# Optimization experiments

Measured on AMD Instinct MI355X. Metric: run time of the kernel, lower is better.

The kernel has to match this reference:

```python
import jax, jax.numpy as jnp
import numpy as np

N, E, R = 50000, 400000, 500
X_SIZE = 100
G_SIZE = 100
HID = 64
OUT = 64
HEADS = 2
ALPHA = 0.5
NEG_SLOPE = 0.01  # nn.LeakyReLU default and attention slope
EPS = 1e-12       # F.normalize eps


def _l2norm(x, axis):
    return x / jnp.maximum(jnp.linalg.norm(x, axis=axis, keepdims=True), EPS)


def _xavier(key, shape, gain=1.414):
    fan_in, fan_out = shape[-1], int(np.prod(shape[:-1]))
    std = gain * np.sqrt(2.0 / (fan_in + fan_out))
    return jax.random.normal(key, shape, dtype=jnp.float32) * std


def _att_layer(h, g, row, col, etype, W, b, att, out_size):
    # h: [N, D_h], g: [R, D_g], W: [heads*out, 2*D_h+D_g], att: [1, heads, out]
    n = h.shape[0]
    h_ijk = jnp.concatenate([h[row], h[col], g[etype]], axis=1)      # [E, 2D_h+D_g]
    c_ijk = (h_ijk @ W.T + b).reshape(-1, HEADS, out_size)           # [E, H, O]
    a = jnp.sum(att * c_ijk, axis=2, keepdims=True)                  # [E, H, 1]
    e = jnp.exp(jax.nn.leaky_relu(a, NEG_SLOPE))                     # unnormalized (matches torch exp w/o max-sub)
    denom = jax.ops.segment_sum(e, row, num_segments=n)              # [N, H, 1]
    alpha = e / denom[row]
    # self-edge zeros contribute nothing; segment_sum over num_segments=n is equivalent
    return jax.ops.segment_sum(alpha * c_ijk, col, num_segments=n)   # [N, H, O]


def setup_inputs() -> dict:
    key = jax.random.key(0)
    ks = jax.random.split(key, 20)
    x = jax.random.normal(ks[0], (N, X_SIZE), dtype=jnp.float32)
    g = jax.random.normal(ks[1], (R, G_SIZE), dtype=jnp.float32)
    edge_idx = jax.random.randint(ks[2], (2, E), 0, N)
    edge_type = jax.random.randint(ks[3], (E,), 0, R)
    d1 = 2 * X_SIZE + G_SIZE
    d2 = 2 * HID * HEADS + G_SIZE
    inp = {
        "x": x, "g": g, "edge_idx": edge_idx, "edge_type": edge_type,
        "W1i": _xavier(ks[4], (HEADS * HID, d1)), "b1i": jnp.zeros((HEADS * HID,), jnp.float32),
        "a1i": _xavier(ks[5], (1, HEADS, HID)),
        "W1o": _xavier(ks[6], (HEADS * HID, d1)), "b1o": jnp.zeros((HEADS * HID,), jnp.float32),
        "a1o": _xavier(ks[7], (1, HEADS, HID)),
        "W2i": _xavier(ks[8], (HEADS * OUT, d2)), "b2i": jnp.zeros((HEADS * OUT,), jnp.float32),
        "a2i": _xavier(ks[9], (1, HEADS, OUT)),
        "W2o": _xavier(ks[10], (HEADS * OUT, d2)), "b2o": jnp.zeros((HEADS * OUT,), jnp.float32),
        "a2o": _xavier(ks[11], (1, HEADS, OUT)),
        "We": _xavier(ks[12], (HID, X_SIZE)), "be": jnp.zeros((HID,), jnp.float32),
        "Wr": _xavier(ks[13], (HEADS * HID, G_SIZE)), "br": jnp.zeros((HEADS * HID,), jnp.float32),
    }
    return inp


def reference(x, g, edge_idx, edge_type, W1i, b1i, a1i, W1o, b1o, a1o,
              W2i, b2i, a2i, W2o, b2o, a2o, We, be, Wr, br):
    # x = F.normalize(x, dim=1).detach()
    xn = jax.lax.stop_gradient(_l2norm(x, axis=1))
    row, col = edge_idx[0], edge_idx[1]

    h_in = _att_layer(xn, g, row, col, edge_type, W1i, b1i, a1i, HID)
    h_out = _att_layer(xn, g, col, row, edge_type, W1o, b1o, a1o, HID)
    h = jax.nn.leaky_relu(ALPHA * h_in + (1.0 - ALPHA) * h_out, NEG_SLOPE)
    h = _l2norm(h, axis=2)                                # [N, H, HID]
    h = h.transpose(0, 1, 2).reshape(N, HEADS * HID)      # concat heads

    h_in = _att_layer(h, g, row, col, edge_type, W2i, b2i, a2i, OUT)
    h_out = _att_layer(h, g, col, row, edge_type, W2o, b2o, a2o, OUT)
    h = jax.nn.leaky_relu(ALPHA * h_in + (1.0 - ALPHA) * h_out, NEG_SLOPE)
    h = _l2norm(h, axis=2)                                # [N, H, OUT]

    # EntityLayer: Linear(x)[:, None, :] + h  (requires HID == OUT)
    h_prime = (xn @ We.T + be)[:, None, :] + h            # [N, H, OUT]
    h_prime = h_prime.reshape(N, HEADS * OUT)
    h_prime = _l2norm(h_prime, axis=1)                    # (torch dim=2 bug -> last dim)
    # _merge_heads stores mean but returns input unchanged

    g_prime = g @ Wr.T + br                               # [R, HEADS*HID]
    return h_prime, g_prime
```

## Files before the change

### kernel.cpp

```cpp
#include <hip/hip_runtime.h>

typedef unsigned short u16;
typedef unsigned int u32;
typedef short short8v __attribute__((ext_vector_type(8)));
typedef float float4v __attribute__((ext_vector_type(4)));

#define N_NODES 50000
#define E_EDGES 400000
#define R_REL   500
#define NKEYS   100000
#define SCAN_B  98
#define SEG     ((size_t)N_NODES * 128)

__device__ __forceinline__ float bl(u32 u){ return __uint_as_float(u << 16); }
__device__ __forceinline__ float bh(u32 u){ return __uint_as_float(u & 0xffff0000u); }
__device__ __forceinline__ u16 f2b(float f){
    u32 u = __float_as_uint(f);
    return (u16)((u + 0x7fffu + ((u >> 16) & 1u)) >> 16);
}
__device__ __forceinline__ u32 pk2(float a, float b){ return (u32)f2b(a) | ((u32)f2b(b) << 16); }
__device__ __forceinline__ float lrelu(float x){ return x > 0.f ? x : 0.01f * x; }

__global__ void k_norm_x(const float* __restrict__ x, u16* __restrict__ xnb){
    int wid = threadIdx.x >> 6, l = threadIdx.x & 63;
    int n = blockIdx.x * 4 + wid;
    if (n >= N_NODES) return;
    float v0 = x[(size_t)n * 100 + l];
    float v1 = (l + 64 < 100) ? x[(size_t)n * 100 + 64 + l] : 0.f;
    float ss = v0 * v0 + v1 * v1;
    #pragma unroll
    for (int m = 32; m; m >>= 1) ss += __shfl_xor(ss, m);
    float s = 1.f / fmaxf(sqrtf(ss), 1e-12f);
    xnb[(size_t)n * 128 + l] = f2b(v0 * s);
    xnb[(size_t)n * 128 + 64 + l] = (l + 64 < 100) ? f2b(v1 * s) : (u16)0;
}

__global__ void k_build_wcat(const float* __restrict__ W1i, const float* __restrict__ W1o,
                             const float* __restrict__ W2i, const float* __restrict__ W2o,
                             const float* __restrict__ We,
                             const float* __restrict__ a1i, const float* __restrict__ a1o,
                             const float* __restrict__ a2i, const float* __restrict__ a2o,
                             u16* __restrict__ wc1, u16* __restrict__ wc2,
                             float* __restrict__ attcat){
    int idx = blockIdx.x * blockDim.x + threadIdx.x;
    if (idx < 576 * 128){
        int r = idx >> 7, k = idx & 127;
        float v = 0.f;
        if (r < 512){
            int seg = r >> 7, rr = r & 127;
            const float* W = (seg < 2) ? W1i : W1o;
            int off = (seg & 1) ? 100 : 0;
            if (k < 100) v = W[(size_t)rr * 300 + off + k];
        } else {
            int rr = r - 512;
            if (k < 100) v = We[(size_t)rr * 100 + k];
        }
        wc1[idx] = f2b(v);
    } else if (idx < 576 * 128 + 512 * 128){
        int j = idx - 576 * 128;
        int r = j >> 7, k = j & 127;
        int seg = r >> 7, rr = r & 127;
        const float* W = (seg < 2) ? W2i : W2o;
        int off = (seg & 1) ? 128 : 0;
        wc2[j] = f2b(W[(size_t)rr * 356 + off + k]);
    } else if (idx < 576 * 128 + 512 * 128 + 1024){
        int j = idx - (576 * 128 + 512 * 128);
        int s = j >> 9, cc = j & 511;
        const float* a = s ? ((cc < 256) ? a2i : a2o) : ((cc < 256) ? a1i : a1o);
        attcat[j] = a[cc & 127];
    }
}

__global__ void k_pg(const float* __restrict__ g,
                     const float* __restrict__ W1i, const float* __restrict__ W1o,
                     const float* __restrict__ W2i, const float* __restrict__ W2o,
                     const float* __restrict__ b1i, const float* __restrict__ b1o,
                     const float* __restrict__ b2i, const float* __restrict__ b2o,
                     const float* __restrict__ a1i, const float* __restrict__ a1o,
                     const float* __restrict__ a2i, const float* __restrict__ a2o,
                     float* __restrict__ Pg, float* __restrict__ qg){
    int bid = blockIdx.x;
    int r = bid >> 2, t = bid & 3;
    const float *W, *b, *att; int ld, off;
    if (t == 0){ W = W1i; ld = 300; off = 200; b = b1i; att = a1i; }
    else if (t == 1){ W = W1o; ld = 300; off = 200; b = b1o; att = a1o; }
    else if (t == 2){ W = W2i; ld = 356; off = 256; b = b2i; att = a2i; }
    else { W = W2o; ld = 356; off = 256; b = b2o; att = a2o; }
    __shared__ float gs[100];
    __shared__ float red[128];
    int j = threadIdx.x;
    if (j < 100) gs[j] = g[(size_t)r * 100 + j];
    __syncthreads();
    float acc = b[j];
    #pragma unroll 4
    for (int k = 0; k < 100; ++k) acc += gs[k] * W[(size_t)j * ld + off + k];
    Pg[((size_t)t * R_REL + r) * 128 + j] = acc;
    red[j] = att[j] * acc;
    __syncthreads();
    if (j < 2){
        float s = 0.f;
        for (int k = 0; k < 64; ++k) s += red[j * 64 + k];
        qg[((size_t)t * R_REL + r) * 2 + j] = s;
    }
}

__global__ void k_gprime(const float* __restrict__ g, const float* __restrict__ Wr,
                         const float* __restrict__ br, float* __restrict__ out){
    int r = blockIdx.x, j = threadIdx.x;
    __shared__ float gs[100];
    if (j < 100) gs[j] = g[(size_t)r * 100 + j];
    __syncthreads();
    float acc = br[j];
    #pragma unroll 4
    for (int k = 0; k < 100; ++k) acc += gs[k] * Wr[(size_t)j * 100 + k];
    out[(size_t)N_NODES * 128 + (size_t)r * 128 + j] = acc;
}

__launch_bounds__(256)
__global__ void k_gemm(const u16* __restrict__ A, const u16* __restrict__ W,
                       const float* __restrict__ attcat,
                       u16* __restrict__ NPt, float* __restrict__ q, int M, int NN){
    int l = threadIdx.x & 63, w = threadIdx.x >> 6;
    int rb = blockIdx.x * 64 + w * 16;
    int ar = rb + (l & 15); if (ar >= M) ar = M - 1;
    const u16* Ap = A + (size_t)ar * 128 + (l >> 4) * 8;
    short8v a0 = *(const short8v*)(Ap);
    short8v a1 = *(const short8v*)(Ap + 32);
    short8v a2 = *(const short8v*)(Ap + 64);
    short8v a3 = *(const short8v*)(Ap + 96);
    float qa[4] = {0.f, 0.f, 0.f, 0.f};
    int ntc = NN >> 4;
    for (int nt = 0; nt < ntc; ++nt){
        const u16* Wp = W + (size_t)(nt * 16 + (l & 15)) * 128 + (l >> 4) * 8;
        short8v b0 = *(const short8v*)(Wp);
        short8v b1 = *(const short8v*)(Wp + 32);
        short8v b2 = *(const short8v*)(Wp + 64);
        short8v b3 = *(const short8v*)(Wp + 96);
        float4v acc = {0.f, 0.f, 0.f, 0.f};
        acc = __builtin_amdgcn_mfma_f32_16x16x32_bf16(a0, b0, acc, 0, 0, 0);
        acc = __builtin_amdgcn_mfma_f32_16x16x32_bf16(a1, b1, acc, 0, 0, 0);
        acc = __builtin_amdgcn_mfma_f32_16x16x32_bf16(a2, b2, acc, 0, 0, 0);
        acc = __builtin_amdgcn_mfma_f32_16x16x32_bf16(a3, b3, acc, 0, 0, 0);
        int cc = nt * 16 + (l & 15);
        int seg = cc >> 7;
        int rr0 = rb + (l >> 4) * 4;
        #pragma unroll
        for (int r = 0; r < 4; ++r){
            int rr = rr0 + r;
            if (rr < M){
                if (seg < 4) NPt[(size_t)seg * SEG + (size_t)rr * 128 + (cc & 127)] = f2b(acc[r]);
                else         NPt[4 * SEG + (size_t)rr * 64 + (cc & 63)] = f2b(acc[r]);
            }
        }
        int g = nt >> 2;
        if (g < 8){
            float av = attcat[cc];
            #pragma unroll
            for (int r = 0; r < 4; ++r) qa[r] += av * acc[r];
            if ((nt & 3) == 3){
                #pragma unroll
                for (int r = 0; r < 4; ++r){
                    float s = qa[r];
                    s += __shfl_xor(s, 1); s += __shfl_xor(s, 2);
                    s += __shfl_xor(s, 4); s += __shfl_xor(s, 8);
                    if ((l & 15) == 0){
                        int rr = rr0 + r;
                        if (rr < M) q[(size_t)rr * 8 + g] = s;
                    }
                    qa[r] = 0.f;
                }
            }
        }
    }
}

__global__ void k_hist(const int* __restrict__ ei, u32* __restrict__ cnt){
    int e = blockIdx.x * blockDim.x + threadIdx.x;
    if (e >= E_EDGES) return;
    atomicAdd(&cnt[ei[E_EDGES + e]], 1u);
    atomicAdd(&cnt[N_NODES + ei[e]], 1u);
}

__launch_bounds__(1024)
__global__ void k_scan1(const u32* __restrict__ cnt, u32* __restrict__ off, u32* __restrict__ bsum){
    __shared__ u32 sh[1024];
    int t = threadIdx.x, b = blockIdx.x, idx = b * 1024 + t;
    u32 v = cnt[idx];
    sh[t] = v; __syncthreads();
    #pragma unroll
    for (int d = 1; d < 1024; d <<= 1){
        u32 add = (t >= d) ? sh[t - d] : 0;
        __syncthreads();
        sh[t] += add;
        __syncthreads();
    }
    off[idx] = sh[t] - v;
    if (t == 1023) bsum[b] = sh[1023];
}

__global__ void k_scan2(u32* __restrict__ bsum){
    if (threadIdx.x == 0){
        u32 run = 0;
        for (int i = 0; i < SCAN_B; ++i){ u32 t = bsum[i]; bsum[i] = run; run += t; }
    }
}

__launch_bounds__(1024)
__global__ void k_scan3(u32* __restrict__ off, const u32* __restrict__ bsum){
    int idx = blockIdx.x * 1024 + threadIdx.x;
    off[idx] += bsum[blockIdx.x];
}

__global__ void k_pos(const int* __restrict__ ei, const int* __restrict__ ety,
                      u32* __restrict__ cur,
                      u32* __restrict__ Pso, u32* __restrict__ Pss){
    int e = blockIdx.x * blockDim.x + threadIdx.x;
    if (e >= E_EDGES) return;
    u32 row = (u32)ei[e], col = (u32)ei[E_EDGES + e];
    u32 etb = (u32)ety[e] << 20;
    u32 pI = atomicAdd(&cur[col], 1u);
    Pso[pI] = row | etb;  Pss[pI] = col;
    u32 pO = atomicAdd(&cur[N_NODES + row], 1u);
    Pso[pO] = col | etb;  Pss[pO] = row;
}

__global__ void k_edgeA(const u32* __restrict__ Pso, const u32* __restrict__ Pss,
                        const float* __restrict__ q,
                        const float* __restrict__ qgI, const float* __restrict__ qgO,
                        float2* __restrict__ exI, float2* __restrict__ exO){
    int p = blockIdx.x * blockDim.x + threadIdx.x;
    if (p >= 2 * E_EDGES) return;
    u32 so = Pso[p], self = Pss[p];
    u32 oth = so & 0xFFFFF, et = so >> 20;
    u32 row, col;
    if (p < E_EDGES){ row = oth; col = self; } else { row = self; col = oth; }
    const float* qr = q + (size_t)row * 8;
    const float* qc = q + (size_t)col * 8;
    float2 ri, ro;
    ri.x = expf(lrelu(qr[0] + qc[2] + qgI[(size_t)et * 2 + 0]));
    ri.y = expf(lrelu(qr[1] + qc[3] + qgI[(size_t)et * 2 + 1]));
    ro.x = expf(lrelu(qc[4] + qr[6] + qgO[(size_t)et * 2 + 0]));
    ro.y = expf(lrelu(qc[5] + qr[7] + qgO[(size_t)et * 2 + 1]));
    exI[p] = ri;
    exO[p] = ro;
}

__global__ void k_denom(const u32* __restrict__ off,
                        const float2* __restrict__ exI, const float2* __restrict__ exO,
                        float* __restrict__ rdI, float* __restrict__ rdO){
    int n = blockIdx.x * blockDim.x + threadIdx.x;
    if (n >= N_NODES) return;
    float s0 = 0.f, s1 = 0.f;
    for (u32 p = off[N_NODES + n]; p < off[N_NODES + n + 1]; ++p){
        float2 v = exI[p]; s0 += v.x; s1 += v.y;
    }
    rdI[(size_t)n * 2 + 0] = (s0 > 0.f) ? 1.f / s0 : 0.f;
    rdI[(size_t)n * 2 + 1] = (s1 > 0.f) ? 1.f / s1 : 0.f;
    float t0 = 0.f, t1 = 0.f;
    for (u32 p = off[n]; p < off[n + 1]; ++p){
        float2 v = exO[p]; t0 += v.x; t1 += v.y;
    }
    rdO[(size_t)n * 2 + 0] = (t0 > 0.f) ? 1.f / t0 : 0.f;
    rdO[(size_t)n * 2 + 1] = (t1 > 0.f) ? 1.f / t1 : 0.f;
}

__launch_bounds__(256)
__global__ void k_agg(const u32* __restrict__ off,
                      const u32* __restrict__ Pso,
                      const float2* __restrict__ exI, const float2* __restrict__ exO,
                      const u16* __restrict__ NPt,
                      const float* __restrict__ PgI, const float* __restrict__ PgO,
                      const float* __restrict__ rdI, const float* __restrict__ rdO,
                      int final_stage,
                      const u16* __restrict__ NPt1, const float* __restrict__ be,
                      u16* __restrict__ h1b, float* __restrict__ out){
    int wid = threadIdx.x >> 6, l = threadIdx.x & 63;
    int n = blockIdx.x * 4 + wid;
    if (n >= N_NODES) return;
    int h = l >> 5, d0 = l * 2;
    const u16* PaI = NPt;
    const u16* PbI = NPt + SEG;
    const u16* PaO = NPt + 2 * SEG;
    const u16* PbO = NPt + 3 * SEG;
    u32 pbi = *(const u32*)(PbI + (size_t)n * 128 + d0);
    u32 pbo = *(const u32*)(PbO + (size_t)n * 128 + d0);

    float a0 = 0.f, a1 = 0.f, sai = 0.f;
    {
        u32 s0 = off[n], deg = off[n + 1] - s0;
        for (u32 base = 0; base < deg; base += 64){
            u32 k = base + (u32)l;
            u32 so = 0u; float w0 = 0.f, w1 = 0.f;
            if (k < deg){
                u32 idx = s0 + k;
                so = __builtin_nontemporal_load(Pso + idx);
                const float* ep = (const float*)exI + (size_t)idx * 2;
                float e0 = __builtin_nontemporal_load(ep);
                float e1 = __builtin_nontemporal_load(ep + 1);
                u32 oth = so & 0xFFFFFu;
                float2 rd2 = *(const float2*)(rdI + (size_t)oth * 2);
                w0 = e0 * rd2.x; w1 = e1 * rd2.y;
            }
            int cnt = (int)((deg - base < 64u) ? (deg - base) : 64u);
            for (int c = 0; c < cnt; c += 8){
                float wj[8]; u32 pa[8]; float2 gv[8];
                #pragma unroll
                for (int j = 0; j < 8; ++j){
                    u32 s = __shfl(so, c + j);
                    float v0 = __shfl(w0, c + j);
                    float v1 = __shfl(w1, c + j);
                    u32 oth = s & 0xFFFFFu, et = s >> 20;
                    pa[j] = *(const u32*)(PaI + (size_t)oth * 128 + d0);
                    gv[j] = *(const float2*)(PgI + (size_t)et * 128 + d0);
                    wj[j] = h ? v1 : v0;
                }
                #pragma unroll
                for (int j = 0; j < 8; ++j){
                    a0 += wj[j] * (bl(pa[j]) + gv[j].x);
                    a1 += wj[j] * (bh(pa[j]) + gv[j].y);
                    sai += wj[j];
                }
            }
        }
    }
    a0 += sai * bl(pbi);
    a1 += sai * bh(pbi);

    float b0 = 0.f, b1 = 0.f, sao = 0.f;
    {
        u32 s0 = off[N_NODES + n], deg = off[N_NODES + n + 1] - s0;
        for (u32 base = 0; base < deg; base += 64){
            u32 k = base + (u32)l;
            u32 so = 0u; float w0 = 0.f, w1 = 0.f;
            if (k < deg){
                u32 idx = s0 + k;
                so = __builtin_nontemporal_load(Pso + idx);
                const float* ep = (const float*)exO + (size_t)idx * 2;
                float e0 = __builtin_nontemporal_load(ep);
                float e1 = __builtin_nontemporal_load(ep + 1);
                u32 oth = so & 0xFFFFFu;
                float2 rd2 = *(const float2*)(rdO + (size_t)oth * 2);
                w0 = e0 * rd2.x; w1 = e1 * rd2.y;
            }
            int cnt = (int)((deg - base < 64u) ? (deg - base) : 64u);
            for (int c = 0; c < cnt; c += 8){
                float wj[8]; u32 pa[8]; float2 gv[8];
                #pragma unroll
                for (int j = 0; j < 8; ++j){
                    u32 s = __shfl(so, c + j);
                    float v0 = __shfl(w0, c + j);
                    float v1 = __shfl(w1, c + j);
                    u32 oth = s & 0xFFFFFu, et = s >> 20;
                    pa[j] = *(const u32*)(PaO + (size_t)oth * 128 + d0);
                    gv[j] = *(const float2*)(PgO + (size_t)et * 128 + d0);
                    wj[j] = h ? v1 : v0;
                }
                #pragma unroll
                for (int j = 0; j < 8; ++j){
                    b0 += wj[j] * (bl(pa[j]) + gv[j].x);
                    b1 += wj[j] * (bh(pa[j]) + gv[j].y);
                    sao += wj[j];
                }
            }
        }
    }
    b0 += sao * bl(pbo);
    b1 += sao * bh(pbo);

    float vx = lrelu(0.5f * (a0 + b0));
    float vy = lrelu(0.5f * (a1 + b1));
    float ss = vx * vx + vy * vy;
    #pragma unroll
    for (int m = 16; m; m >>= 1) ss += __shfl_xor(ss, m);
    float s2 = 1.f / fmaxf(sqrtf(ss), 1e-12f);
    if (!final_stage){
        *(u32*)(h1b + (size_t)n * 128 + d0) = pk2(vx * s2, vy * s2);
    } else {
        float h20 = vx * s2, h21 = vy * s2;
        int o0 = d0 & 63;
        u32 ue = *(const u32*)(NPt1 + 4 * SEG + (size_t)n * 64 + o0);
        float hp0 = bl(ue) + be[o0] + h20;
        float hp1 = bh(ue) + be[o0 + 1] + h21;
        float st = hp0 * hp0 + hp1 * hp1;
        #pragma unroll
        for (int m = 32; m; m >>= 1) st += __shfl_xor(st, m);
        float s = 1.f / fmaxf(sqrtf(st), 1e-12f);
        float2 o; o.x = hp0 * s; o.y = hp1 * s;
        *(float2*)(out + (size_t)n * 128 + d0) = o;
    }
}

extern "C" void kernel_launch(void* const* d_in, const int* in_sizes, int n_in,
                              void* d_out, int out_size, void* d_ws, size_t ws_size,
                              hipStream_t stream){
    const float* x   = (const float*)d_in[0];
    const float* g   = (const float*)d_in[1];
    const int*   ei  = (const int*)d_in[2];
    const int*   ety = (const int*)d_in[3];
    const float* W1i = (const float*)d_in[4];
    const float* b1i = (const float*)d_in[5];
    const float* a1i = (const float*)d_in[6];
    const float* W1o = (const float*)d_in[7];
    const float* b1o = (const float*)d_in[8];
    const float* a1o = (const float*)d_in[9];
    const float* W2i = (const float*)d_in[10];
    const float* b2i = (const float*)d_in[11];
    const float* a2i = (const float*)d_in[12];
    const float* W2o = (const float*)d_in[13];
    const float* b2o = (const float*)d_in[14];
    const float* a2o = (const float*)d_in[15];
    const float* We  = (const float*)d_in[16];
    const float* be  = (const float*)d_in[17];
    const float* Wr  = (const float*)d_in[18];
    const float* br  = (const float*)d_in[19];
    float* out = (float*)d_out;

    char* ws = (char*)d_ws;
    size_t off_b = 0;
    auto carve = [&](size_t bytes) -> char* {
        char* p = ws + off_b;
        off_b += (bytes + 255) & ~(size_t)255;
        return p;
    };
    u16*    xnb   = (u16*)carve((size_t)N_NODES * 128 * 2);
    u16*    wc1   = (u16*)carve((size_t)576 * 128 * 2);
    u16*    wc2   = (u16*)carve((size_t)512 * 128 * 2);
    float*  attct = (float*)carve((size_t)1024 * 4);
    u16*    NPt1  = (u16*)carve((SEG * 4 + (size_t)N_NODES * 64) * 2);
    u16*    NPt2  = (u16*)carve(SEG * 4 * 2);
    u16*    h1b   = (u16*)carve((size_t)N_NODES * 128 * 2);
    float*  q     = (float*)carve((size_t)N_NODES * 8 * 4);
    float*  Pg    = (float*)carve((size_t)4 * R_REL * 128 * 4);
    float*  qg    = (float*)carve((size_t)4 * R_REL * 2 * 4);
    u32*    cnt   = (u32*)carve((size_t)SCAN_B * 1024 * 4);
    u32*    offA  = (u32*)carve((size_t)SCAN_B * 1024 * 4);
    u32*    cur   = (u32*)carve((size_t)NKEYS * 4);
    u32*    bsum  = (u32*)carve((size_t)SCAN_B * 4);
    u32*    Pso   = (u32*)carve((size_t)2 * E_EDGES * 4);
    u32*    Pss   = (u32*)carve((size_t)2 * E_EDGES * 4);
    float2* exI   = (float2*)carve((size_t)2 * E_EDGES * 8);
    float2* exO   = (float2*)carve((size_t)2 * E_EDGES * 8);
    float*  rdI   = (float*)carve((size_t)N_NODES * 2 * 4);
    float*  rdO   = (float*)carve((size_t)N_NODES * 2 * 4);

    hipMemsetAsync(cnt, 0, (size_t)SCAN_B * 1024 * 4, stream);
    k_hist<<<1563, 256, 0, stream>>>(ei, cnt);
    k_scan1<<<SCAN_B, 1024, 0, stream>>>(cnt, offA, bsum);
    k_scan2<<<1, 64, 0, stream>>>(bsum);
    k_scan3<<<SCAN_B, 1024, 0, stream>>>(offA, bsum);
    hipMemcpyAsync(cur, offA, (size_t)NKEYS * 4, hipMemcpyDeviceToDevice, stream);
    k_pos<<<1563, 256, 0, stream>>>(ei, ety, cur, Pso, Pss);

    k_norm_x<<<12500, 256, 0, stream>>>(x, xnb);
    k_build_wcat<<<548, 256, 0, stream>>>(W1i, W1o, W2i, W2o, We,
                                          a1i, a1o, a2i, a2o, wc1, wc2, attct);
    k_pg<<<2000, 128, 0, stream>>>(g, W1i, W1o, W2i, W2o, b1i, b1o, b2i, b2o,
                                   a1i, a1o, a2i, a2o, Pg, qg);
    k_gprime<<<500, 128, 0, stream>>>(g, Wr, br, out);

    k_gemm<<<782, 256, 0, stream>>>(xnb, wc1, attct, NPt1, q, N_NODES, 576);
    k_edgeA<<<3125, 256, 0, stream>>>(Pso, Pss, q, qg, qg + R_REL * 2, exI, exO);
    k_denom<<<196, 256, 0, stream>>>(offA, exI, exO, rdI, rdO);
    k_agg<<<12500, 256, 0, stream>>>(offA, Pso, exI, exO, NPt1, Pg, Pg + R_REL * 128,
                                     rdI, rdO, 0, NPt1, be, h1b, out);

    k_gemm<<<782, 256, 0, stream>>>(h1b, wc2, attct + 512, NPt2, q, N_NODES, 512);
    k_edgeA<<<3125, 256, 0, stream>>>(Pso, Pss, q, qg + 2 * R_REL * 2, qg + 3 * R_REL * 2,
                                      exI, exO);
    k_denom<<<196, 256, 0, stream>>>(offA, exI, exO, rdI, rdO);
    k_agg<<<12500, 256, 0, stream>>>(offA, Pso, exI, exO, NPt2, Pg + 2 * R_REL * 128,
                                     Pg + 3 * R_REL * 128, rdI, rdO, 1, NPt1, be, h1b, out);
}
```

Before: 437.4 us.

## Split GEMM columns across grid y and stage outputs through LDS for coalesced stores

The node GEMM kernel now launches a second grid dimension, with each block handling one 128-column group instead of looping over all output columns. Results are staged in padded shared memory per wave and then written to global memory as 16-byte vectors, replacing scattered 2-byte stores. This targets poor store coalescing and low parallelism in the GEMM. The cost is that the A tile is reloaded once per column group, and the kernel adds a block-wide synchronisation.

```diff
diff --git a/kernel.cpp b/kernel.cpp
--- a/kernel.cpp
+++ b/kernel.cpp
@@ -120,8 +120,17 @@
 __global__ void k_gemm(const u16* __restrict__ A, const u16* __restrict__ W,
                        const float* __restrict__ attcat,
                        u16* __restrict__ NPt, float* __restrict__ q, int M, int NN){
+    __shared__ __align__(16) char lds[4 * 16 * 272];
     int l = threadIdx.x & 63, w = threadIdx.x >> 6;
     int rb = blockIdx.x * 64 + w * 16;
+    int grp = blockIdx.y;
+    int cb = grp * 128;
+    int ncols = NN - cb; if (ncols > 128) ncols = 128;
+    int tiles = ncols >> 4;
+    int rowW = (ncols == 128) ? 128 : 64;
+    int pitch = rowW * 2 + 16;
+    char* lw = lds + w * 16 * pitch;
+
     int ar = rb + (l & 15); if (ar >= M) ar = M - 1;
     const u16* Ap = A + (size_t)ar * 128 + (l >> 4) * 8;
     short8v a0 = *(const short8v*)(Ap);
@@ -129,9 +138,11 @@
     short8v a2 = *(const short8v*)(Ap + 64);
     short8v a3 = *(const short8v*)(Ap + 96);
     float qa[4] = {0.f, 0.f, 0.f, 0.f};
-    int ntc = NN >> 4;
-    for (int nt = 0; nt < ntc; ++nt){
-        const u16* Wp = W + (size_t)(nt * 16 + (l & 15)) * 128 + (l >> 4) * 8;
+    bool doq = (cb < 512);
+    int rloc0 = (l >> 4) * 4;
+    for (int t = 0; t < tiles; ++t){
+        int cc = cb + t * 16 + (l & 15);
+        const u16* Wp = W + (size_t)cc * 128 + (l >> 4) * 8;
         short8v b0 = *(const short8v*)(Wp);
         short8v b1 = *(const short8v*)(Wp + 32);
         short8v b2 = *(const short8v*)(Wp + 64);
@@ -141,35 +152,41 @@
         acc = __builtin_amdgcn_mfma_f32_16x16x32_bf16(a1, b1, acc, 0, 0, 0);
         acc = __builtin_amdgcn_mfma_f32_16x16x32_bf16(a2, b2, acc, 0, 0, 0);
         acc = __builtin_amdgcn_mfma_f32_16x16x32_bf16(a3, b3, acc, 0, 0, 0);
-        int cc = nt * 16 + (l & 15);
-        int seg = cc >> 7;
-        int rr0 = rb + (l >> 4) * 4;
+        int lcol = t * 16 + (l & 15);
         #pragma unroll
-        for (int r = 0; r < 4; ++r){
-            int rr = rr0 + r;
-            if (rr < M){
-                if (seg < 4) NPt[(size_t)seg * SEG + (size_t)rr * 128 + (cc & 127)] = f2b(acc[r]);
-                else         NPt[4 * SEG + (size_t)rr * 64 + (cc & 63)] = f2b(acc[r]);
-            }
-        }
-        int g = nt >> 2;
-        if (g < 8){
+        for (int r = 0; r < 4; ++r)
+            *(u16*)(lw + (size_t)(rloc0 + r) * pitch + lcol * 2) = f2b(acc[r]);
+        if (doq){
             float av = attcat[cc];
             #pragma unroll
             for (int r = 0; r < 4; ++r) qa[r] += av * acc[r];
-            if ((nt & 3) == 3){
+            if ((t & 3) == 3){
+                int g = (cb >> 6) + (t >> 2);
                 #pragma unroll
                 for (int r = 0; r < 4; ++r){
                     float s = qa[r];
                     s += __shfl_xor(s, 1); s += __shfl_xor(s, 2);
                     s += __shfl_xor(s, 4); s += __shfl_xor(s, 8);
                     if ((l & 15) == 0){
-                        int rr = rr0 + r;
+                        int rr = rb + rloc0 + r;
                         if (rr < M) q[(size_t)rr * 8 + g] = s;
                     }
                     qa[r] = 0.f;
                 }
             }
+        }
+    }
+    __syncthreads();
+    u16* gb = (rowW == 128) ? (NPt + (size_t)grp * SEG + (size_t)rb * 128)
+                            : (NPt + 4 * SEG + (size_t)rb * 64);
+    int chunks = (rowW == 128) ? 4 : 2;
+    for (int i = 0; i < chunks; ++i){
+        int u = i * 512 + l * 8;
+        int rloc = (rowW == 128) ? (u >> 7) : (u >> 6);
+        int c    = (rowW == 128) ? (u & 127) : (u & 63);
+        if (rb + rloc < M){
+            short8v v = *(const short8v*)(lw + (size_t)rloc * pitch + c * 2);
+            *(short8v*)(gb + u) = v;
         }
     }
 }
@@ -458,13 +475,13 @@
                                    a1i, a1o, a2i, a2o, Pg, qg);
     k_gprime<<<500, 128, 0, stream>>>(g, Wr, br, out);
 
-    k_gemm<<<782, 256, 0, stream>>>(xnb, wc1, attct, NPt1, q, N_NODES, 576);
+    k_gemm<<<dim3(782, 5), 256, 0, stream>>>(xnb, wc1, attct, NPt1, q, N_NODES, 576);
     k_edgeA<<<3125, 256, 0, stream>>>(Pso, Pss, q, qg, qg + R_REL * 2, exI, exO);
     k_denom<<<196, 256, 0, stream>>>(offA, exI, exO, rdI, rdO);
     k_agg<<<12500, 256, 0, stream>>>(offA, Pso, exI, exO, NPt1, Pg, Pg + R_REL * 128,
                                      rdI, rdO, 0, NPt1, be, h1b, out);
 
-    k_gemm<<<782, 256, 0, stream>>>(h1b, wc2, attct + 512, NPt2, q, N_NODES, 512);
+    k_gemm<<<dim3(782, 4), 256, 0, stream>>>(h1b, wc2, attct + 512, NPt2, q, N_NODES, 512);
     k_edgeA<<<3125, 256, 0, stream>>>(Pso, Pss, q, qg + 2 * R_REL * 2, qg + 3 * R_REL * 2,
                                       exI, exO);
     k_denom<<<196, 256, 0, stream>>>(offA, exI, exO, rdI, rdO);
```

Result: faster. 425.5 us (-2.7%).
